# Optimization experiments

Hardware: AMD Instinct MI355X
Metric: run time of the kernel (lower is better)

## Reference

```python
import jax, jax.numpy as jnp
import numpy as np

B_SZ, SEQ_LEN, STATE_DIM, D_IN, D_OUT, KX = 8, 2048, 1024, 512, 512, 10


def setup_inputs() -> dict:
    key = jax.random.key(0)
    ks = jax.random.split(key, 7)
    inputs = jax.random.normal(ks[0], (B_SZ, SEQ_LEN, D_IN), dtype=jnp.float32)
    h0 = jax.random.normal(ks[1], (STATE_DIM,), dtype=jnp.float32)
    # exponential_decay_init(lam=15): x = clamp(-1/lam * log(1-u), max=1); A = (1-x)*sign
    u = jax.random.uniform(ks[2], (STATE_DIM,), dtype=jnp.float32)
    x = jnp.minimum(-(1.0 / 15.0) * jnp.log1p(-u), 1.0)
    sign = jnp.sign(jax.random.normal(ks[3], (STATE_DIM,), dtype=jnp.float32))
    A = (1.0 - x) * sign
    Bm = jax.random.normal(ks[4], (D_IN, STATE_DIM), dtype=jnp.float32) / D_IN
    C = jax.random.normal(ks[5], (STATE_DIM, D_OUT), dtype=jnp.float32) / STATE_DIM
    M = jax.random.normal(ks[6], (D_OUT, D_IN, KX), dtype=jnp.float32) / D_OUT
    return {"inputs": inputs, "h0": h0, "A": A, "B": Bm, "C": C, "M": M}


def _ar_preds(M, x):
    # Equivalent to einsum('oik,bli->bklo') + per-k roll + triu mask + sum over k:
    # ar[b,l,:] = sum_{i=0}^{k-1, i<=l} M[:,:,i] @ x[b, l-i, :]
    b, l, d_in = x.shape
    kx = M.shape[2]
    ar = jnp.einsum('oi,bli->blo', M[:, :, 0], x)
    for i in range(1, kx):
        x_shift = jnp.pad(x, ((0, 0), (i, 0), (0, 0)))[:, :l]  # shift right, zero-fill
        ar = ar + jnp.einsum('oi,bli->blo', M[:, :, i], x_shift)
    return ar


def reference(inputs, h0, A, B, C, M):
    b, l, d_in = inputs.shape
    state_dim = A.shape[0]
    # Project inputs once: u_t @ B for all t -> [b, l, s]
    uB = jnp.einsum('bli,is->bls', inputs, B)

    def step(h, u_t):
        h = A * h + u_t  # diagonal recurrence
        return h, h

    h_init = jnp.broadcast_to(h0, (b, state_dim))
    _, hs = jax.lax.scan(step, h_init, jnp.swapaxes(uB, 0, 1))  # [l, b, s]
    hs = jnp.swapaxes(hs, 0, 1)  # [b, l, s]
    lds_out = hs @ C  # [b, l, d_out]
    return lds_out + _ar_preds(M, inputs)
```

## Files before the change

### kernel.cpp

```cpp
#include <hip/hip_runtime.h>

#define B_SZ   8
#define SEQ    2048
#define PSEQ   (SEQ+16)
#define SDIM   1024
#define DIN    512
#define DOUT   512
#define KX     10
#define RTOT   (B_SZ*SEQ)
#define LC     64
#define NC     (SEQ/LC)

typedef __attribute__((ext_vector_type(8))) short short8;
typedef __attribute__((ext_vector_type(4))) float f32x4;
typedef __attribute__((ext_vector_type(4))) unsigned short bfx4;

#define OFF_XP   0UL
#define OFF_UB   16908288UL
#define OFF_HS   50462720UL
#define OFF_BT   84017152UL
#define OFF_CT   85065728UL
#define OFF_MT   86114304UL

__device__ __forceinline__ short f2bf(float f) {
  unsigned u = __builtin_bit_cast(unsigned, f);
  u += 0x7fffu + ((u >> 16) & 1u);
  return (short)(u >> 16);
}
__device__ __forceinline__ float bf2f(unsigned short b) {
  return __builtin_bit_cast(float, (unsigned)b << 16);
}

#define GLOAD16(gp, lp) __builtin_amdgcn_global_load_lds( \
    (const __attribute__((address_space(1))) void*)(gp), \
    (__attribute__((address_space(3))) void*)(lp), 16, 0, 0)
#define WAITVM(n) asm volatile("s_waitcnt vmcnt(" #n ")" ::: "memory")
#define SBAR() __builtin_amdgcn_s_barrier()

__global__ void k_conv_x(const float* __restrict__ in, short* __restrict__ out) {
  const int NG = RTOT * (DIN / 8);
  for (int g = blockIdx.x * 256 + threadIdx.x; g < NG; g += 2048 * 256) {
    int r = g >> 6, c8 = g & 63;
    int b = r >> 11, t = r & 2047;
    const float4* p = reinterpret_cast<const float4*>(in) + (size_t)g * 2;
    float4 f0 = p[0], f1 = p[1];
    short8 o;
    o[0]=f2bf(f0.x); o[1]=f2bf(f0.y); o[2]=f2bf(f0.z); o[3]=f2bf(f0.w);
    o[4]=f2bf(f1.x); o[5]=f2bf(f1.y); o[6]=f2bf(f1.z); o[7]=f2bf(f1.w);
    *reinterpret_cast<short8*>(out + ((size_t)(b * PSEQ + 16 + t) * DIN + c8 * 8)) = o;
  }
}

__global__ void k_zero_pad(short* __restrict__ Xp) {
  int idx = blockIdx.x * 256 + threadIdx.x;
  if (idx >= B_SZ * 16 * (DIN / 8)) return;
  int b = idx >> 10, rem = idx & 1023;
  int row16 = rem >> 6, c8 = rem & 63;
  const short8 z = {0,0,0,0,0,0,0,0};
  *reinterpret_cast<short8*>(Xp + ((size_t)(b * PSEQ + row16) * DIN + c8 * 8)) = z;
}

__global__ void k_transpose_bf16(const float* __restrict__ in, short* __restrict__ out,
                                 int rows, int cols) {
  __shared__ float t[32][33];
  int bx = blockIdx.x * 32, by = blockIdx.y * 32;
  int tx = threadIdx.x & 31, ty = threadIdx.x >> 5;
  #pragma unroll
  for (int j = 0; j < 32; j += 8)
    t[ty + j][tx] = in[(size_t)(by + ty + j) * cols + (bx + tx)];
  __syncthreads();
  #pragma unroll
  for (int j = 0; j < 32; j += 8)
    out[(size_t)(bx + ty + j) * rows + (by + tx)] = f2bf(t[tx][ty + j]);
}

__global__ void k_prep_M(const float* __restrict__ M, short* __restrict__ Mt) {
  int idx = blockIdx.x * 256 + threadIdx.x;
  if (idx >= DOUT * DIN) return;
  int o = idx / DIN, i = idx - o * DIN;
  const float* src = M + ((size_t)o * DIN + i) * KX;
  #pragma unroll
  for (int t = 0; t < KX; ++t)
    Mt[((size_t)t * DOUT + o) * DIN + i] = f2bf(src[t]);
}

__global__ void k_scan_E(const short* __restrict__ uB, const float* __restrict__ A,
                         float* __restrict__ E) {
  int blk = blockIdx.x, tid = threadIdx.x;
  int b = blk >> 5, c = blk & 31;
  int s0 = tid * 4;
  const short* base = uB + ((size_t)b * SEQ + (size_t)c * LC) * SDIM + s0;
  float a[4], h[4];
  #pragma unroll
  for (int j = 0; j < 4; ++j) { a[j] = A[s0 + j]; h[j] = 0.f; }
  for (int t = 0; t < LC; ++t) {
    bfx4 v = *reinterpret_cast<const bfx4*>(base + (size_t)t * SDIM);
    #pragma unroll
    for (int j = 0; j < 4; ++j) h[j] = fmaf(a[j], h[j], bf2f(v[j]));
  }
  float* ep = E + (size_t)blk * SDIM + s0;
  #pragma unroll
  for (int j = 0; j < 4; ++j) ep[j] = h[j];
}

__global__ void k_scan_S(const float* __restrict__ E, const float* __restrict__ A,
                         const float* __restrict__ h0, float* __restrict__ Sb) {
  int blk = blockIdx.x, tid = threadIdx.x;
  int b = blk >> 2;
  int s = ((blk & 3) << 8) + tid;
  float a = A[s], ap = a;
  #pragma unroll
  for (int q = 0; q < 6; ++q) ap *= ap;
  float S = h0[s];
  for (int c = 0; c < NC; ++c) {
    size_t idx = ((size_t)b * NC + c) * SDIM + s;
    Sb[idx] = S;
    S = fmaf(ap, S, E[idx]);
  }
}

__global__ void k_scan_h(const short* __restrict__ uB, const float* __restrict__ A,
                         const float* __restrict__ Sb, short* __restrict__ hs) {
  int blk = blockIdx.x, tid = threadIdx.x;
  int b = blk >> 5, c = blk & 31;
  int s0 = tid * 4;
  const short* base = uB + ((size_t)b * SEQ + (size_t)c * LC) * SDIM + s0;
  short* hbase = hs + ((size_t)b * SEQ + (size_t)c * LC) * SDIM + s0;
  float a[4], h[4];
  #pragma unroll
  for (int j = 0; j < 4; ++j) {
    a[j] = A[s0 + j];
    h[j] = Sb[(size_t)blk * SDIM + s0 + j];
  }
  for (int t = 0; t < LC; ++t) {
    bfx4 v = *reinterpret_cast<const bfx4*>(base + (size_t)t * SDIM);
    bfx4 o;
    #pragma unroll
    for (int j = 0; j < 4; ++j) {
      h[j] = fmaf(a[j], h[j], bf2f(v[j]));
      o[j] = (unsigned short)f2bf(h[j]);
    }
    *reinterpret_cast<bfx4*>(hbase + (size_t)t * SDIM) = o;
  }
}

__device__ __forceinline__ void stage128(const short* __restrict__ g, int ld,
                                         short* l, int tid) {
  int rsub = tid >> 3;
  int slot = (tid & 7) ^ (rsub & 7);
  #pragma unroll
  for (int i = 0; i < 4; ++i) {
    int row = i * 32 + rsub;
    GLOAD16(g + (size_t)row * ld + slot * 8, l + row * 64 + (tid & 7) * 8);
  }
}

__device__ __forceinline__ void mfma_tile(const short* lA, int aoff, const short* lB,
                                          int lane, int wm, int wn, f32x4 acc[4][4]) {
  int lr = lane & 15;
  int h  = lane >> 4;
  #pragma unroll
  for (int kk = 0; kk < 2; ++kk) {
    int kslot = kk * 4 + h;
    short8 af[4], bfr[4];
    #pragma unroll
    for (int mi = 0; mi < 4; ++mi) {
      int row = aoff + wm * 64 + mi * 16 + lr;
      af[mi] = *reinterpret_cast<const short8*>(lA + row * 64 + ((kslot ^ (row & 7)) << 3));
    }
    #pragma unroll
    for (int ni = 0; ni < 4; ++ni) {
      int row = wn * 64 + ni * 16 + lr;
      bfr[ni] = *reinterpret_cast<const short8*>(lB + row * 64 + ((kslot ^ (row & 7)) << 3));
    }
    __builtin_amdgcn_s_setprio(1);
    #pragma unroll
    for (int mi = 0; mi < 4; ++mi)
      #pragma unroll
      for (int ni = 0; ni < 4; ++ni)
        acc[mi][ni] = __builtin_amdgcn_mfma_f32_16x16x32_bf16(af[mi], bfr[ni], acc[mi][ni], 0, 0, 0);
    __builtin_amdgcn_s_setprio(0);
  }
}

__global__ __launch_bounds__(256) void k_gemm_uB(const short* __restrict__ Xp,
                                                 const short* __restrict__ Bt,
                                                 short* __restrict__ uB) {
  __shared__ __attribute__((aligned(16))) short lds[32768];
  short* A0 = lds;         short* B0 = lds + 8192;
  short* A1 = lds + 16384; short* B1 = lds + 24576;
  int tid = threadIdx.x, lane = tid & 63, w = tid >> 6, wm = w >> 1, wn = w & 1;
  long r0 = (long)blockIdx.x * 128;
  int  c0 = blockIdx.y * 128;
  int  b  = (int)(r0 >> 11);
  const short* Abase = Xp + (size_t)(r0 + 16 * (b + 1)) * DIN;
  const short* Bbase = Bt + (size_t)c0 * DIN;
  const f32x4 z4 = {0.f, 0.f, 0.f, 0.f};
  f32x4 acc[4][4];
  #pragma unroll
  for (int mi = 0; mi < 4; ++mi)
    #pragma unroll
    for (int ni = 0; ni < 4; ++ni) acc[mi][ni] = z4;

  stage128(Abase, DIN, A0, tid);      stage128(Bbase, DIN, B0, tid);
  stage128(Abase + 64, DIN, A1, tid); stage128(Bbase + 64, DIN, B1, tid);
  WAITVM(8);
  SBAR();
  for (int kt = 0; kt < 8; ++kt) {
    const short* a  = (kt & 1) ? A1 : A0;
    const short* bb = (kt & 1) ? B1 : B0;
    mfma_tile(a, 0, bb, lane, wm, wn, acc);
    SBAR();
    if (kt + 2 < 8) {
      short* ad = (kt & 1) ? A1 : A0;
      short* bd = (kt & 1) ? B1 : B0;
      stage128(Abase + (kt + 2) * 64, DIN, ad, tid);
      stage128(Bbase + (kt + 2) * 64, DIN, bd, tid);
      WAITVM(8);
    } else {
      WAITVM(0);
    }
    SBAR();
  }
  #pragma unroll
  for (int mi = 0; mi < 4; ++mi)
    #pragma unroll
    for (int ni = 0; ni < 4; ++ni)
      #pragma unroll
      for (int r = 0; r < 4; ++r) {
        long row = r0 + wm * 64 + mi * 16 + (lane >> 4) * 4 + r;
        int  col = c0 + wn * 64 + ni * 16 + (lane & 15);
        uB[(size_t)row * SDIM + col] = f2bf(acc[mi][ni][r]);
      }
}


__device__ __forceinline__ void stageA256(const short* __restrict__ g, int ld,
                                          short* l, int tid) {
  int rsub = tid >> 3;
  int slot = (tid & 7) ^ (rsub & 7);
  #pragma unroll
  for (int i = 0; i < 4; ++i) {
    int row = i * 64 + rsub;
    GLOAD16(g + (size_t)row * ld + slot * 8, l + row * 64 + (tid & 7) * 8);
  }
}
__device__ __forceinline__ void stageB128(const short* __restrict__ g, int ld,
                                          short* l, int tid) {
  int rsub = tid >> 3;
  int slot = (tid & 7) ^ (rsub & 7);
  #pragma unroll
  for (int i = 0; i < 2; ++i) {
    int row = i * 64 + rsub;
    GLOAD16(g + (size_t)row * ld + slot * 8, l + row * 64 + (tid & 7) * 8);
  }
}
__device__ __forceinline__ void stageX272(const short* __restrict__ g, int ld,
                                          short* l, int tid) {
  stageA256(g, ld, l, tid);
  if (tid < 128) {
    int rsub = tid >> 3;
    int row = 256 + rsub;
    int slot = (tid & 7) ^ (row & 7);
    GLOAD16(g + (size_t)row * ld + slot * 8, l + row * 64 + (tid & 7) * 8);
  }
}

__device__ __forceinline__ void compute_step(const short* la, int aoff, const short* lb,
                                             int lane, int wm, int wn, f32x4 acc[4][4]) {
  int lr = lane & 15;
  int h  = lane >> 4;
  short8 af[4][2], bfr[4][2];
  #pragma unroll
  for (int kk = 0; kk < 2; ++kk) {
    int kslot = kk * 4 + h;
    #pragma unroll
    for (int mi = 0; mi < 4; ++mi) {
      int row = aoff + wm * 64 + mi * 16 + lr;
      af[mi][kk] = *reinterpret_cast<const short8*>(la + row * 64 + ((kslot ^ (row & 7)) << 3));
    }
    #pragma unroll
    for (int ni = 0; ni < 4; ++ni) {
      int row = wn * 64 + ni * 16 + lr;
      bfr[ni][kk] = *reinterpret_cast<const short8*>(lb + row * 64 + ((kslot ^ (row & 7)) << 3));
    }
  }
  __builtin_amdgcn_s_setprio(1);
  #pragma unroll
  for (int kk = 0; kk < 2; ++kk)
    #pragma unroll
    for (int mi = 0; mi < 4; ++mi)
      #pragma unroll
      for (int ni = 0; ni < 4; ++ni)
        acc[mi][ni] = __builtin_amdgcn_mfma_f32_16x16x32_bf16(af[mi][kk], bfr[ni][kk], acc[mi][ni], 0, 0, 0);
  __builtin_amdgcn_s_setprio(0);
}

__global__ __launch_bounds__(512) void k_gemm_out(const short* __restrict__ hs,
                                                  const short* __restrict__ Xp,
                                                  const short* __restrict__ Ct,
                                                  const short* __restrict__ Mt,
                                                  float* __restrict__ out) {
  __shared__ __attribute__((aligned(16))) short lds[51200];
  short* A0p = lds;          short* B0p = lds + 16384;
  short* A1p = lds + 24576;  short* B1p = lds + 40960;
  short* Xs0 = lds;          short* Xs1 = lds + 17408;
  short* M0p = lds + 34816;  short* M1p = lds + 43008;
  int tid = threadIdx.x, lane = tid & 63, w = tid >> 6;
  int wm = w >> 1, wn = w & 1;
  int bid = blockIdx.x;
  int sw  = (bid & 7) * 32 + (bid >> 3);
  long r0 = (long)(sw & 63) * 256;
  int  c0 = (sw >> 6) * 128;
  int  b  = (int)(r0 >> 11);
  const short* hsA = hs + (size_t)r0 * SDIM;
  const short* CtB = Ct + (size_t)c0 * SDIM;
  const short* Xa  = Xp + (size_t)(r0 + 16 * (b + 1) - 16) * DIN;
  const short* MtB = Mt + (size_t)c0 * DIN;

  const f32x4 z4 = {0.f, 0.f, 0.f, 0.f};
  f32x4 acc[4][4];
  #pragma unroll
  for (int mi = 0; mi < 4; ++mi)
    #pragma unroll
    for (int ni = 0; ni < 4; ++ni) acc[mi][ni] = z4;

  stageA256(hsA, SDIM, A0p, tid);
  stageB128(CtB, SDIM, B0p, tid);
  stageA256(hsA + 64, SDIM, A1p, tid);
  stageB128(CtB + 64, SDIM, B1p, tid);
  WAITVM(6);
  SBAR();
  for (int s = 0; s < 16; ++s) {
    const short* la = (s & 1) ? A1p : A0p;
    const short* lb = (s & 1) ? B1p : B0p;
    compute_step(la, 0, lb, lane, wm, wn, acc);
    SBAR();
    if (s + 2 < 16) {
      short* na = (s & 1) ? A1p : A0p;
      short* nb = (s & 1) ? B1p : B0p;
      stageA256(hsA + (s + 2) * 64, SDIM, na, tid);
      stageB128(CtB + (s + 2) * 64, SDIM, nb, tid);
      WAITVM(6);
    } else if (s == 14) {
      stageX272(Xa, DIN, Xs0, tid);
      WAITVM(4);
    } else {
      stageB128(MtB, DIN, M0p, tid);
      stageB128(MtB + (size_t)DOUT * DIN, DIN, M1p, tid);
      WAITVM(2);
    }
    SBAR();
  }

  for (int k0 = 0; k0 < 8; ++k0) {
    const short* xs = (k0 & 1) ? Xs1 : Xs0;
    short*       xn = (k0 & 1) ? Xs0 : Xs1;
    int kc = k0 * 64;
    bool lastslice = (k0 == 7);
    for (int j = 0; j < KX; ++j) {
      const short* lm = (j & 1) ? M1p : M0p;
      short*       nm = (j & 1) ? M1p : M0p;
      compute_step(xs, 16 - j, lm, lane, wm, wn, acc);
      SBAR();
      if (j + 2 < KX)
        stageB128(MtB + (size_t)(j + 2) * DOUT * DIN + kc, DIN, nm, tid);
      else if (!lastslice)
        stageB128(MtB + (size_t)(j + 2 - KX) * DOUT * DIN + kc + 64, DIN, nm, tid);
      if (j == 1 && !lastslice)
        stageX272(Xa + kc + 64, DIN, xn, tid);
      if ((j == 1 || j == 2) && !lastslice) {
        WAITVM(6);
      } else if (j + 2 < KX || !lastslice) {
        WAITVM(2);
      } else {
        WAITVM(0);
      }
      SBAR();
    }
  }

  #pragma unroll
  for (int mi = 0; mi < 4; ++mi)
    #pragma unroll
    for (int ni = 0; ni < 4; ++ni)
      #pragma unroll
      for (int r = 0; r < 4; ++r) {
        long row = r0 + wm * 64 + mi * 16 + (lane >> 4) * 4 + r;
        int  col = c0 + wn * 64 + ni * 16 + (lane & 15);
        out[(size_t)row * DOUT + col] = acc[mi][ni][r];
      }
}

extern "C" void kernel_launch(void* const* d_in, const int* in_sizes, int n_in,
                              void* d_out, int out_size, void* d_ws, size_t ws_size,
                              hipStream_t stream) {
  (void)in_sizes; (void)n_in; (void)out_size; (void)ws_size;
  const float* x  = (const float*)d_in[0];
  const float* h0 = (const float*)d_in[1];
  const float* A  = (const float*)d_in[2];
  const float* B  = (const float*)d_in[3];
  const float* C  = (const float*)d_in[4];
  const float* M  = (const float*)d_in[5];
  float* out = (float*)d_out;
  char* ws = (char*)d_ws;

  short* Xp  = (short*)(ws + OFF_XP);
  short* uB  = (short*)(ws + OFF_UB);
  short* hsb = (short*)(ws + OFF_HS);
  short* Bt  = (short*)(ws + OFF_BT);
  short* Ct  = (short*)(ws + OFF_CT);
  short* Mt  = (short*)(ws + OFF_MT);
  float* E   = out;
  float* Sb  = out + B_SZ * NC * SDIM;

  k_conv_x<<<2048, 256, 0, stream>>>(x, Xp);
  k_zero_pad<<<32, 256, 0, stream>>>(Xp);
  k_transpose_bf16<<<dim3(SDIM / 32, DIN / 32), 256, 0, stream>>>(B, Bt, DIN, SDIM);
  k_transpose_bf16<<<dim3(DOUT / 32, SDIM / 32), 256, 0, stream>>>(C, Ct, SDIM, DOUT);
  k_prep_M<<<(DOUT * DIN + 255) / 256, 256, 0, stream>>>(M, Mt);

  k_gemm_uB<<<dim3(RTOT / 128, SDIM / 128), 256, 0, stream>>>(Xp, Bt, uB);

  k_scan_E<<<B_SZ * NC, 256, 0, stream>>>(uB, A, E);
  k_scan_S<<<B_SZ * 4, 256, 0, stream>>>(E, A, h0, Sb);
  k_scan_h<<<B_SZ * NC, 256, 0, stream>>>(uB, A, Sb, hsb);

  k_gemm_out<<<256, 512, 0, stream>>>(hsb, Xp, Ct, Mt, out);
}
```

Baseline: 156.0 us.

## Triple-buffer LDS stages and prefetch MFMA fragments in output GEMM

Restructures k_gemm_out's main loop to triple-buffer global→LDS stages (hs/C and M tiles) and to double-buffer register fragments. The LDS reads for the next step are interleaved with the current step's MFMAs through sched_group_barrier. X staging grows to 320 rows and the workspace offsets shift to match. The aim is to hide LDS read and global load latency behind MFMA work, at the cost of more LDS (160KB), more registers, and a launch-bounds hint of 2 blocks per CU that may not be achievable.

```diff
diff --git a/kernel.cpp b/kernel.cpp
--- a/kernel.cpp
+++ b/kernel.cpp
@@ -16,11 +16,11 @@
 typedef __attribute__((ext_vector_type(4))) unsigned short bfx4;
 
 #define OFF_XP   0UL
-#define OFF_UB   16908288UL
-#define OFF_HS   50462720UL
-#define OFF_BT   84017152UL
-#define OFF_CT   85065728UL
-#define OFF_MT   86114304UL
+#define OFF_UB   16973824UL
+#define OFF_HS   50528256UL
+#define OFF_BT   84082688UL
+#define OFF_CT   85131264UL
+#define OFF_MT   86179840UL
 
 __device__ __forceinline__ short f2bf(float f) {
   unsigned u = __builtin_bit_cast(unsigned, f);
@@ -35,6 +35,8 @@
     (const __attribute__((address_space(1))) void*)(gp), \
     (__attribute__((address_space(3))) void*)(lp), 16, 0, 0)
 #define WAITVM(n) asm volatile("s_waitcnt vmcnt(" #n ")" ::: "memory")
+#define LGKM0()   do { asm volatile("s_waitcnt lgkmcnt(0)" ::: "memory"); \
+                       __builtin_amdgcn_sched_barrier(0); } while (0)
 #define SBAR() __builtin_amdgcn_s_barrier()
 
 __global__ void k_conv_x(const float* __restrict__ in, short* __restrict__ out) {
@@ -235,6 +237,45 @@
 }
 
 
+struct Frags { short8 a[4][2]; short8 b[4][2]; };
+
+__device__ __forceinline__ void read_frags(Frags& f, const short* la, int aoff,
+                                           const short* lb, int lane, int wm, int wn) {
+  int lr = lane & 15, h = lane >> 4;
+  #pragma unroll
+  for (int kk = 0; kk < 2; ++kk) {
+    int kslot = kk * 4 + h;
+    #pragma unroll
+    for (int mi = 0; mi < 4; ++mi) {
+      int row = aoff + wm * 64 + mi * 16 + lr;
+      f.a[mi][kk] = *reinterpret_cast<const short8*>(la + row * 64 + ((kslot ^ (row & 7)) << 3));
+    }
+    #pragma unroll
+    for (int ni = 0; ni < 4; ++ni) {
+      int row = wn * 64 + ni * 16 + lr;
+      f.b[ni][kk] = *reinterpret_cast<const short8*>(lb + row * 64 + ((kslot ^ (row & 7)) << 3));
+    }
+  }
+}
+
+__device__ __forceinline__ void mfma_frags(const Frags& f, f32x4 acc[4][4]) {
+  #pragma unroll
+  for (int kk = 0; kk < 2; ++kk)
+    #pragma unroll
+    for (int mi = 0; mi < 4; ++mi)
+      #pragma unroll
+      for (int ni = 0; ni < 4; ++ni)
+        acc[mi][ni] = __builtin_amdgcn_mfma_f32_16x16x32_bf16(f.a[mi][kk], f.b[ni][kk], acc[mi][ni], 0, 0, 0);
+}
+
+__device__ __forceinline__ void sgb_interleave() {
+  #pragma unroll
+  for (int i = 0; i < 16; ++i) {
+    __builtin_amdgcn_sched_group_barrier(0x008, 2, 0);
+    __builtin_amdgcn_sched_group_barrier(0x100, 1, 0);
+  }
+}
+
 __device__ __forceinline__ void stageA256(const short* __restrict__ g, int ld,
                                           short* l, int tid) {
   int rsub = tid >> 3;
@@ -255,57 +296,31 @@
     GLOAD16(g + (size_t)row * ld + slot * 8, l + row * 64 + (tid & 7) * 8);
   }
 }
-__device__ __forceinline__ void stageX272(const short* __restrict__ g, int ld,
+__device__ __forceinline__ void stageX320(const short* __restrict__ g,
                                           short* l, int tid) {
-  stageA256(g, ld, l, tid);
-  if (tid < 128) {
-    int rsub = tid >> 3;
-    int row = 256 + rsub;
-    int slot = (tid & 7) ^ (row & 7);
-    GLOAD16(g + (size_t)row * ld + slot * 8, l + row * 64 + (tid & 7) * 8);
-  }
-}
-
-__device__ __forceinline__ void compute_step(const short* la, int aoff, const short* lb,
-                                             int lane, int wm, int wn, f32x4 acc[4][4]) {
-  int lr = lane & 15;
-  int h  = lane >> 4;
-  short8 af[4][2], bfr[4][2];
-  #pragma unroll
-  for (int kk = 0; kk < 2; ++kk) {
-    int kslot = kk * 4 + h;
-    #pragma unroll
-    for (int mi = 0; mi < 4; ++mi) {
-      int row = aoff + wm * 64 + mi * 16 + lr;
-      af[mi][kk] = *reinterpret_cast<const short8*>(la + row * 64 + ((kslot ^ (row & 7)) << 3));
-    }
-    #pragma unroll
-    for (int ni = 0; ni < 4; ++ni) {
-      int row = wn * 64 + ni * 16 + lr;
-      bfr[ni][kk] = *reinterpret_cast<const short8*>(lb + row * 64 + ((kslot ^ (row & 7)) << 3));
-    }
-  }
-  __builtin_amdgcn_s_setprio(1);
-  #pragma unroll
-  for (int kk = 0; kk < 2; ++kk)
-    #pragma unroll
-    for (int mi = 0; mi < 4; ++mi)
-      #pragma unroll
-      for (int ni = 0; ni < 4; ++ni)
-        acc[mi][ni] = __builtin_amdgcn_mfma_f32_16x16x32_bf16(af[mi][kk], bfr[ni][kk], acc[mi][ni], 0, 0, 0);
-  __builtin_amdgcn_s_setprio(0);
-}
-
-__global__ __launch_bounds__(512) void k_gemm_out(const short* __restrict__ hs,
-                                                  const short* __restrict__ Xp,
-                                                  const short* __restrict__ Ct,
-                                                  const short* __restrict__ Mt,
-                                                  float* __restrict__ out) {
-  __shared__ __attribute__((aligned(16))) short lds[51200];
-  short* A0p = lds;          short* B0p = lds + 16384;
-  short* A1p = lds + 24576;  short* B1p = lds + 40960;
-  short* Xs0 = lds;          short* Xs1 = lds + 17408;
-  short* M0p = lds + 34816;  short* M1p = lds + 43008;
+  int rsub = tid >> 3;
+  int slot = (tid & 7) ^ (rsub & 7);
+  #pragma unroll
+  for (int i = 0; i < 5; ++i) {
+    int row = i * 64 + rsub;
+    GLOAD16(g + (size_t)row * DIN + slot * 8, l + row * 64 + (tid & 7) * 8);
+  }
+}
+
+__global__ __launch_bounds__(512, 2) void k_gemm_out(const short* __restrict__ hs,
+                                                     const short* __restrict__ Xp,
+                                                     const short* __restrict__ Ct,
+                                                     const short* __restrict__ Mt,
+                                                     float* __restrict__ out) {
+  __shared__ __attribute__((aligned(16))) short lds[81920];
+  short* const P0  = lds;
+  short* const P1  = lds + 24576;
+  short* const P2  = lds + 49152;
+  short* const Xs0 = lds;
+  short* const Xs1 = lds + 20480;
+  short* const PM0 = lds + 57344;
+  short* const PM1 = lds + 65536;
+  short* const PM2 = lds + 73728;
   int tid = threadIdx.x, lane = tid & 63, w = tid >> 6;
   int wm = w >> 1, wn = w & 1;
   int bid = blockIdx.x;
@@ -325,56 +340,82 @@
     #pragma unroll
     for (int ni = 0; ni < 4; ++ni) acc[mi][ni] = z4;
 
-  stageA256(hsA, SDIM, A0p, tid);
-  stageB128(CtB, SDIM, B0p, tid);
-  stageA256(hsA + 64, SDIM, A1p, tid);
-  stageB128(CtB + 64, SDIM, B1p, tid);
+  Frags fr[2];
+
+  stageA256(hsA,        SDIM, P0, tid);  stageB128(CtB,        SDIM, P0 + 16384, tid);
+  stageA256(hsA + 64,   SDIM, P1, tid);  stageB128(CtB + 64,   SDIM, P1 + 16384, tid);
+  stageA256(hsA + 128,  SDIM, P2, tid);  stageB128(CtB + 128,  SDIM, P2 + 16384, tid);
   WAITVM(6);
   SBAR();
+  read_frags(fr[0], P0, 0, P0 + 16384, lane, wm, wn);
+
+  #pragma unroll
   for (int s = 0; s < 16; ++s) {
-    const short* la = (s & 1) ? A1p : A0p;
-    const short* lb = (s & 1) ? B1p : B0p;
-    compute_step(la, 0, lb, lane, wm, wn, acc);
+    __builtin_amdgcn_s_setprio(1);
+    mfma_frags(fr[s & 1], acc);
+    if (s < 15) {
+      const short* nb = ((s + 1) % 3 == 0) ? P0 : ((s + 1) % 3 == 1) ? P1 : P2;
+      read_frags(fr[(s + 1) & 1], nb, 0, nb + 16384, lane, wm, wn);
+    } else {
+      read_frags(fr[0], Xs0, 16, PM0, lane, wm, wn);
+    }
+    sgb_interleave();
+    __builtin_amdgcn_s_setprio(0);
+    LGKM0();
     SBAR();
-    if (s + 2 < 16) {
-      short* na = (s & 1) ? A1p : A0p;
-      short* nb = (s & 1) ? B1p : B0p;
-      stageA256(hsA + (s + 2) * 64, SDIM, na, tid);
-      stageB128(CtB + (s + 2) * 64, SDIM, nb, tid);
+    if (s <= 12) {
+      short* sp = (s % 3 == 0) ? P0 : (s % 3 == 1) ? P1 : P2;
+      stageA256(hsA + (s + 3) * 64, SDIM, sp, tid);
+      stageB128(CtB + (s + 3) * 64, SDIM, sp + 16384, tid);
       WAITVM(6);
+    } else if (s == 13) {
+      stageB128(MtB, DIN, PM0, tid);
+      stageB128(MtB + (size_t)DOUT * DIN, DIN, PM1, tid);
+      WAITVM(4);
     } else if (s == 14) {
-      stageX272(Xa, DIN, Xs0, tid);
-      WAITVM(4);
-    } else {
-      stageB128(MtB, DIN, M0p, tid);
-      stageB128(MtB + (size_t)DOUT * DIN, DIN, M1p, tid);
-      WAITVM(2);
+      stageB128(MtB + (size_t)2 * DOUT * DIN, DIN, PM2, tid);
+      stageX320(Xa, Xs0, tid);
+      WAITVM(0);
     }
     SBAR();
   }
 
   for (int k0 = 0; k0 < 8; ++k0) {
+    int kc = k0 * 64;
     const short* xs = (k0 & 1) ? Xs1 : Xs0;
     short*       xn = (k0 & 1) ? Xs0 : Xs1;
-    int kc = k0 * 64;
-    bool lastslice = (k0 == 7);
+    const short* q0 = (k0 % 3 == 0) ? PM0 : (k0 % 3 == 1) ? PM1 : PM2;
+    const short* q1 = (k0 % 3 == 0) ? PM1 : (k0 % 3 == 1) ? PM2 : PM0;
+    const short* q2 = (k0 % 3 == 0) ? PM2 : (k0 % 3 == 1) ? PM0 : PM1;
+    #pragma unroll
     for (int j = 0; j < KX; ++j) {
-      const short* lm = (j & 1) ? M1p : M0p;
-      short*       nm = (j & 1) ? M1p : M0p;
-      compute_step(xs, 16 - j, lm, lane, wm, wn, acc);
+      __builtin_amdgcn_s_setprio(1);
+      mfma_frags(fr[j & 1], acc);
+      bool do_read = (j < 9) || (k0 < 7);
+      if (j < 9) {
+        const short* mn = ((j + 1) % 3 == 0) ? q0 : ((j + 1) % 3 == 1) ? q1 : q2;
+        read_frags(fr[(j + 1) & 1], xs, 15 - j, mn, lane, wm, wn);
+      } else if (k0 < 7) {
+        read_frags(fr[0], xn, 16, q1, lane, wm, wn);
+      }
+      if (do_read) sgb_interleave();
+      __builtin_amdgcn_s_setprio(0);
+      LGKM0();
       SBAR();
-      if (j + 2 < KX)
-        stageB128(MtB + (size_t)(j + 2) * DOUT * DIN + kc, DIN, nm, tid);
-      else if (!lastslice)
-        stageB128(MtB + (size_t)(j + 2 - KX) * DOUT * DIN + kc + 64, DIN, nm, tid);
-      if (j == 1 && !lastslice)
-        stageX272(Xa + kc + 64, DIN, xn, tid);
-      if ((j == 1 || j == 2) && !lastslice) {
-        WAITVM(6);
-      } else if (j + 2 < KX || !lastslice) {
+      if (j + 3 <= 9) {
+        short* mw = (j % 3 == 0) ? (short*)q0 : (j % 3 == 1) ? (short*)q1 : (short*)q2;
+        stageB128(MtB + (size_t)(j + 3) * DOUT * DIN + kc, DIN, mw, tid);
+      } else if (k0 < 7) {
+        short* mw = (j % 3 == 0) ? (short*)q0 : (j % 3 == 1) ? (short*)q1 : (short*)q2;
+        stageB128(MtB + (size_t)(j - 7) * DOUT * DIN + kc + 64, DIN, mw, tid);
+      }
+      if (j == 1 && k0 < 7) stageX320(Xa + kc + 64, xn, tid);
+      if (j == 1 || j == 2) {
+        if (k0 < 7) { WAITVM(7); } else { WAITVM(2); }
+      } else if (j >= 7) {
+        if (k0 == 7) { WAITVM(0); } else { WAITVM(2); }
+      } else {
         WAITVM(2);
-      } else {
-        WAITVM(0);
       }
       SBAR();
     }
```

New measurement: 153.7 us. No clear change (-1.5%).
